# Kernel tuning notes

Measured on AMD Instinct MI355X. Metric: run time of the kernel, lower is better.

The kernel has to match this reference:

```python
import jax, jax.numpy as jnp
import numpy as np
from jax import lax

# 4D convolution (valid padding, stride 1) via XLA's rank-general conv.
# dimension_numbers: N=batch, C=channels, then 4 spatial axes H,W,D,T.
DN = ('NCHWDT', 'OIHWDT', 'NCHWDT')

def conv4d(x, w, b):
    y = lax.conv_general_dilated(x, w, window_strides=(1, 1, 1, 1),
                                 padding='VALID', dimension_numbers=DN)
    return y + b.reshape(1, -1, 1, 1, 1, 1)


def setup_inputs() -> dict:
    key = jax.random.key(0)
    ks = jax.random.split(key, 7)
    B = 128
    x = jax.random.normal(ks[0], (B, 1, 18, 18, 18, 18), dtype=jnp.float32)
    # conv4d(1, 5, 7): weight [out=5, in=1, 7,7,7,7]
    w1 = jax.random.normal(ks[1], (5, 1, 7, 7, 7, 7), dtype=jnp.float32) * 0.02
    b1 = jax.random.normal(ks[2], (5,), dtype=jnp.float32) * 0.02
    # conv4d(5, 10, 7): weight [10, 5, 7,7,7,7]
    w2 = jax.random.normal(ks[3], (10, 5, 7, 7, 7, 7), dtype=jnp.float32) * 0.02
    b2 = jax.random.normal(ks[4], (10,), dtype=jnp.float32) * 0.02
    # Linear(10 * 6**4, 1)
    feat = 10 * 6 ** 4  # 12960
    w_lin = jax.random.normal(ks[5], (1, feat), dtype=jnp.float32) * 0.02
    b_lin = jax.random.normal(ks[6], (1,), dtype=jnp.float32) * 0.02
    return {"x": x, "w1": w1, "b1": b1, "w2": w2, "b2": b2,
            "w_lin": w_lin, "b_lin": b_lin}


def reference(x, w1, b1, w2, b2, w_lin, b_lin):
    # head: conv4d -> ReLU -> conv4d -> ReLU
    h = jax.nn.relu(conv4d(x, w1, b1))          # [B, 5, 12,12,12,12]
    h = jax.nn.relu(conv4d(h, w2, b2))          # [B, 10, 6,6,6,6]
    # out: Flatten -> Dropout(eval: identity) -> Linear -> Sigmoid
    h = h.reshape(h.shape[0], -1)               # [B, 12960]
    logits = h @ w_lin.T + b_lin                 # [B, 1]
    return jax.nn.sigmoid(logits)
```

## Files before the change

### kernel.cpp

```cpp
#include <hip/hip_runtime.h>
#include <math.h>

typedef unsigned u32;
typedef _Float16 f16x8 __attribute__((ext_vector_type(8)));
typedef float    f32x16 __attribute__((ext_vector_type(16)));

static __device__ __forceinline__ u32 pack2(_Float16 a, _Float16 b) {
    union { _Float16 h[2]; u32 u; } v;
    v.h[0] = a; v.h[1] = b;
    return v.u;
}


__global__ __launch_bounds__(256) void pack_A1p(
    const float* __restrict__ w1, _Float16* __restrict__ A1)
{
    int i = blockIdx.x * 256 + threadIdx.x;
    if (i >= 9728) return;
    u32 outv = 0u;
    int kh = i / 1164, r = i % 1164;
    if (kh < 7 && r < 1148) {
        int kw = r / 164, r2 = r % 164;
        if (r2 < 140) {
            int kd = r2 / 20, r3 = r2 % 20;
            int oc = r3 / 4, j2 = r3 % 4;
            int j0 = 2 * j2, j1 = 2 * j2 + 1;
            const float* wb = w1 + oc * 2401 + kh * 343 + kw * 49 + kd * 7;
            _Float16 v0 = (j0 < 7) ? (_Float16)wb[j0] : (_Float16)0.f;
            _Float16 v1 = (j1 < 7) ? (_Float16)wb[j1] : (_Float16)0.f;
            outv = pack2(v0, v1);
        }
    }
    ((u32*)A1)[i] = outv;
}

__global__ __launch_bounds__(256) void pack_A2p(
    const float* __restrict__ w2, _Float16* __restrict__ A2)
{
    int i = blockIdx.x * 256 + threadIdx.x;
    if (i >= 79040) return;
    int ci = i / 15808, r = i % 15808;
    int kh = r / 1976, r2 = r % 1976;
    u32 outv = 0u;
    if (kh < 7 && r2 < 1960) {
        int kw = r2 / 280, r3 = r2 % 280;
        int kd = r3 / 40, r4 = r3 % 40;
        int oc = r4 / 4, j2 = r4 % 4;
        int j0 = 2 * j2, j1 = 2 * j2 + 1;
        const float* wb = w2 + oc * 12005 + ci * 2401 + kh * 343 + kw * 49 + kd * 7;
        _Float16 v0 = (j0 < 7) ? (_Float16)wb[j0] : (_Float16)0.f;
        _Float16 v1 = (j1 < 7) ? (_Float16)wb[j1] : (_Float16)0.f;
        outv = pack2(v0, v1);
    }
    ((u32*)A2)[i] = outv;
}

#define C1_SLAB 9360
#define C1_AOFF 9360
#define C1_LDS  (9360 + 9728)
__global__ __launch_bounds__(256, 2) void conv1_mfma(
    const float* __restrict__ x, const _Float16* __restrict__ A1,
    const float* __restrict__ b1, _Float16* __restrict__ h1)
{
    __shared__ u32 lds[C1_LDS];
    int tid = threadIdx.x;
    int lane = tid & 63;
    int wave = tid >> 6;
    int col = lane & 31;
    int g = lane >> 5;

    int bid = (int)blockIdx.x;
    int lbid = (bid & 7) * 192 + (bid >> 3);
    int OWp = lbid % 3;
    int OH = (lbid / 3) & 3;
    int b = lbid / 12;

    int qn[3], u_[3], od_[3], ot_[3];
    #pragma unroll
    for (int s = 0; s < 3; ++s) {
        int nt = wave + 4 * s;
        int n = (nt <= 8) ? nt * 32 + col : col;
        int u = n / 144, r2 = n % 144;
        int od = r2 / 12, ot = r2 % 12;
        u_[s] = u; od_[s] = od; ot_[s] = ot;
        qn[s] = (u * 36 + od) * 52 + ot * 4;
    }

    f32x16 acc0, acc1, acc2;
    #pragma unroll
    for (int q = 0; q < 16; ++q) { acc0[q] = 0.f; acc1[q] = 0.f; acc2[q] = 0.f; }

    const float* xbase = x + (size_t)b * 104976;
    int w10 = tid / 18, id18 = tid % 18;
    int iw = 4 * OWp + w10;
    bool stager = (tid < 180);

    int mc = (col < 30) ? col : 29;
    int am_dw = mc / 15, am_dh = (mc % 15) / 5, am_oc = mc % 5;
    int jadd = 4 * (col - mc);
    int vlane = 4 * am_oc - 164 * am_dw + jadd;
    int zbase = C1_AOFF + 8312 + vlane;
    bool eLo = (am_dw == 1);
    bool e3  = (am_dw == 1) && (g == 0);
    bool e24 = (am_dw == 0) && (g == 1);
    bool eHi = (am_dw == 0);

    float2 xr[9];
    {
        const uint4* asrc = (const uint4*)A1;
        uint4* adst = (uint4*)(lds + C1_AOFF);
        #pragma unroll
        for (int i = 0; i < 10; ++i) {
            int q = tid + 256 * i;
            if (q < 2432) adst[q] = asrc[q];
        }
        if (stager) {
            const float2* src = (const float2*)(xbase + (3 * OH) * 5832 + iw * 324 + id18 * 18);
            #pragma unroll
            for (int q = 0; q < 9; ++q) xr[q] = src[q];
        }
    }

    for (int se = 0; se < 9; ++se) {
        int kh = se - am_dh;
        int vbase = (kh >= 0 && kh < 7) ? (C1_AOFF + kh * 1164 + vlane) : zbase;

        __syncthreads();
        if (stager) {
            _Float16 h[19];
            #pragma unroll
            for (int q = 0; q < 9; ++q) { h[2*q] = (_Float16)xr[q].x; h[2*q+1] = (_Float16)xr[q].y; }
            h[18] = (_Float16)0.f;
            u32 e[9], o[9];
            #pragma unroll
            for (int q = 0; q < 9; ++q) e[q] = pack2(h[2*q], h[2*q+1]);
            #pragma unroll
            for (int q = 0; q < 9; ++q) o[q] = pack2(h[2*q+1], (q < 8) ? h[2*q+2] : h[18]);
            int base = tid * 52;
            #pragma unroll
            for (int ot = 0; ot < 12; ++ot) {
                uint4 w;
                if ((ot & 1) == 0) { const int q = ot >> 1;   w = (uint4){e[q], e[q+1], e[q+2], e[q+3]}; }
                else               { const int q = (ot-1)>>1; w = (uint4){o[q], o[q+1], o[q+2], o[q+3]}; }
                *(uint4*)(&lds[base + ot * 4]) = w;
            }
        }
        __syncthreads();

        if (se < 8 && stager) {
            const float2* src = (const float2*)(xbase + (3 * OH + se + 1) * 5832 + iw * 324 + id18 * 18);
            #pragma unroll
            for (int q = 0; q < 9; ++q) xr[q] = src[q];
        }

        #pragma unroll
        for (int k2 = 0; k2 < 28; ++k2) {
            const int t0 = 2 * k2, t1 = 2 * k2 + 1;
            const int c0 = ((t0 / 7) * 18 + (t0 % 7)) * 52;
            const int c1 = ((t1 / 7) * 18 + (t1 % 7)) * 52;
            const int ca0 = 164 * (t0 / 7) + 20 * (t0 % 7);
            const int ca1 = 164 * (t1 / 7) + 20 * (t1 % 7);
            int qoff = g ? c1 : c0;
            int ca   = g ? ca1 : ca0;
            int abase;
            if (k2 <= 2)       abase = eLo ? zbase : vbase;
            else if (k2 == 3)  abase = e3  ? zbase : vbase;
            else if (k2 == 24) abase = e24 ? zbase : vbase;
            else if (k2 >= 25) abase = eHi ? zbase : vbase;
            else               abase = vbase;
            f16x8 af = *(const f16x8*)(lds + abase + ca);
            f16x8 bf0 = *(const f16x8*)(lds + qn[0] + qoff);
            f16x8 bf1 = *(const f16x8*)(lds + qn[1] + qoff);
            acc0 = __builtin_amdgcn_mfma_f32_32x32x16_f16(af, bf0, acc0, 0, 0, 0);
            acc1 = __builtin_amdgcn_mfma_f32_32x32x16_f16(af, bf1, acc1, 0, 0, 0);
            if (wave == 0) {
                f16x8 bf2 = *(const f16x8*)(lds + qn[2] + qoff);
                acc2 = __builtin_amdgcn_mfma_f32_32x32x16_f16(af, bf2, acc2, 0, 0, 0);
            }
        }
    }

    #pragma unroll
    for (int s = 0; s < 3; ++s) {
        if (s == 2 && wave != 0) continue;
        f32x16 a = (s == 0) ? acc0 : ((s == 1) ? acc1 : acc2);
        int ow_b = 4 * OWp + 2 * u_[s];
        #pragma unroll
        for (int r = 0; r < 16; ++r) {
            const int m0 = (r & 3) + 8 * (r >> 2);
            const int m1 = m0 + 4;
            const int dw0 = m0 / 15, dh0 = (m0 % 15) / 5, oc0 = m0 % 5;
            const int dw1 = m1 / 15, dh1 = (m1 % 15) / 5, oc1 = m1 % 5;
            if (m1 >= 30 && g) continue;
            int dw = g ? dw1 : dw0;
            int dh = g ? dh1 : dh0;
            int oc = g ? oc1 : oc0;
            float bv = g ? b1[oc1] : b1[oc0];
            float v = fmaxf(a[r] + bv, 0.f);
            h1[(size_t)b * 103680 + oc * 20736 + (3 * OH + dh) * 1728
               + (ow_b + dw) * 144 + od_[s] * 12 + ot_[s]] = (_Float16)v;
        }
    }
}

#define C2_SLAB 4032
#define C2_AOFF 4032
#define C2_LDS  (4032 + 15808)
__global__ __launch_bounds__(256, 2) void conv2_mfma(
    const _Float16* __restrict__ h1, const _Float16* __restrict__ A2,
    _Float16* __restrict__ part)
{
    __shared__ u32 lds[C2_LDS];
    int tid = threadIdx.x;
    int lane = tid & 63;
    int wave = tid >> 6;
    int col = lane & 31;
    int g = lane >> 5;

    int bid = (int)blockIdx.x;
    int lbid = (bid & 7) * 160 + (bid >> 3);
    int ci = lbid % 5;
    int OH2 = (lbid / 5) & 1;
    int b = lbid / 10;

    int qn[2], n_[2];
    #pragma unroll
    for (int s = 0; s < 2; ++s) {
        int nt = wave + 4 * s;
        int n = nt * 32 + col;
        n_[s] = n;
        int nc = (n < 216) ? n : 215;
        int ow = nc / 36, rem = nc % 36;
        int od = rem / 6, ot = rem % 6;
        qn[s] = (ow * 12 + od) * 28 + ot * 4;
    }

    f32x16 acc0, acc1;
    #pragma unroll
    for (int q = 0; q < 16; ++q) { acc0[q] = 0.f; acc1[q] = 0.f; }

    const _Float16* hbase = h1 + (size_t)b * 103680 + ci * 20736;
    int iw = tid / 12, id12 = tid % 12;
    bool stager = (tid < 144);

    int mc = (col < 30) ? col : 29;
    int am_dh = mc / 10, am_oc = mc % 10;
    int jadd = 4 * (col - mc);
    int vlane = 4 * am_oc + jadd;
    int zb = C2_AOFF + 13832 + vlane;

    uint2 xr[3];
    {
        const uint4* asrc = (const uint4*)A2 + (size_t)ci * 3952;
        uint4* adst = (uint4*)(lds + C2_AOFF);
        #pragma unroll
        for (int i = 0; i < 16; ++i) {
            int q = tid + 256 * i;
            if (q < 3952) adst[q] = asrc[q];
        }
        if (stager) {
            const uint2* src = (const uint2*)(hbase + (3 * OH2) * 1728 + iw * 144 + id12 * 12);
            #pragma unroll
            for (int q = 0; q < 3; ++q) xr[q] = src[q];
        }
    }

    for (int she = 0; she < 9; ++she) {
        int kh = she - am_dh;
        int vb = (kh >= 0 && kh < 7) ? (C2_AOFF + kh * 1976 + vlane) : zb;

        __syncthreads();
        if (stager) {
            _Float16 h[14];
            *(uint2*)&h[0] = xr[0]; *(uint2*)&h[4] = xr[1]; *(uint2*)&h[8] = xr[2];
            h[12] = (_Float16)0.f;
            u32 e[6], o[6];
            #pragma unroll
            for (int q = 0; q < 6; ++q) e[q] = pack2(h[2*q], h[2*q+1]);
            #pragma unroll
            for (int q = 0; q < 6; ++q) o[q] = pack2(h[2*q+1], (q < 5) ? h[2*q+2] : h[12]);
            int base = tid * 28;
            #pragma unroll
            for (int ot = 0; ot < 6; ++ot) {
                uint4 w;
                if ((ot & 1) == 0) { const int q = ot >> 1;   w = (uint4){e[q], e[q+1], e[q+2], e[q+3]}; }
                else               { const int q = (ot-1)>>1; w = (uint4){o[q], o[q+1], o[q+2], o[q+3]}; }
                *(uint4*)(&lds[base + ot * 4]) = w;
            }
        }
        __syncthreads();

        if (she < 8 && stager) {
            const uint2* src = (const uint2*)(hbase + (3 * OH2 + she + 1) * 1728 + iw * 144 + id12 * 12);
            #pragma unroll
            for (int q = 0; q < 3; ++q) xr[q] = src[q];
        }

        #pragma unroll
        for (int k2 = 0; k2 < 25; ++k2) {
            const int t0 = 2 * k2, t1 = 2 * k2 + 1;
            const int c0 = ((t0 / 7) * 12 + (t0 % 7)) * 28;
            const int c1 = (t1 < 49) ? ((t1 / 7) * 12 + (t1 % 7)) * 28 : 0;
            const int a0 = 280 * (t0 / 7) + 40 * (t0 % 7);
            const int a1 = (t1 < 49) ? (280 * (t1 / 7) + 40 * (t1 % 7)) : 0;
            int qoff = g ? c1 : c0;
            int ca   = g ? a1 : a0;
            int ab = (k2 == 24 && g) ? zb : vb;
            f16x8 af = *(const f16x8*)(lds + ab + ca);
            f16x8 bf0 = *(const f16x8*)(lds + qn[0] + qoff);
            acc0 = __builtin_amdgcn_mfma_f32_32x32x16_f16(af, bf0, acc0, 0, 0, 0);
            if (wave < 3) {
                f16x8 bf1 = *(const f16x8*)(lds + qn[1] + qoff);
                acc1 = __builtin_amdgcn_mfma_f32_32x32x16_f16(af, bf1, acc1, 0, 0, 0);
            }
        }
    }

    #pragma unroll
    for (int s = 0; s < 2; ++s) {
        if (s == 1 && wave >= 3) continue;
        if (n_[s] >= 216) continue;
        f32x16 a = (s == 0) ? acc0 : acc1;
        #pragma unroll
        for (int r = 0; r < 16; ++r) {
            const int m0 = (r & 3) + 8 * (r >> 2);
            const int m1 = m0 + 4;
            const int dh0 = m0 / 10, oc0 = m0 % 10;
            const int dh1 = m1 / 10, oc1 = m1 % 10;
            if (m1 >= 30 && g) continue;
            int dh = g ? dh1 : dh0;
            int oc = g ? oc1 : oc0;
            int oh = 3 * OH2 + dh;
            part[((size_t)(ci * 768 + b * 6 + oh) * 10 + oc) * 216 + n_[s]] = (_Float16)a[r];
        }
    }
}

__global__ __launch_bounds__(256) void conv2_reduce(
    const _Float16* __restrict__ part, const float* __restrict__ b2,
    _Float16* __restrict__ h2)
{
    int flat = blockIdx.x * 256 + threadIdx.x;
    int n_loc = flat % 216;
    int t = flat / 216;
    int oc = t % 10;  t /= 10;
    int oh = t % 6;
    int b  = t / 6;
    float s = 0.f;
    #pragma unroll
    for (int ci = 0; ci < 5; ++ci)
        s += (float)part[((size_t)(ci * 768 + b * 6 + oh) * 10 + oc) * 216 + n_loc];
    s = fmaxf(s + b2[oc], 0.f);
    h2[(size_t)b * 12960 + oc * 1296 + oh * 216 + n_loc] = (_Float16)s;
}

__global__ __launch_bounds__(256) void linear_kernel(
    const _Float16* __restrict__ h2, const float* __restrict__ wl,
    const float* __restrict__ bl, float* __restrict__ out)
{
    int b = blockIdx.x;
    const _Float16* hb = h2 + (size_t)b * 12960;
    float s = 0.f;
    for (int i = threadIdx.x; i < 12960; i += 256)
        s += (float)hb[i] * wl[i];
    #pragma unroll
    for (int off = 32; off > 0; off >>= 1)
        s += __shfl_down(s, off, 64);
    __shared__ float wsum[4];
    int wave = threadIdx.x >> 6;
    if ((threadIdx.x & 63) == 0) wsum[wave] = s;
    __syncthreads();
    if (threadIdx.x == 0) {
        float tot = wsum[0] + wsum[1] + wsum[2] + wsum[3] + bl[0];
        out[b] = 1.f / (1.f + expf(-tot));
    }
}

extern "C" void kernel_launch(void* const* d_in, const int* in_sizes, int n_in,
                              void* d_out, int out_size, void* d_ws, size_t ws_size,
                              hipStream_t stream) {
    const float* x  = (const float*)d_in[0];
    const float* w1 = (const float*)d_in[1];
    const float* b1 = (const float*)d_in[2];
    const float* w2 = (const float*)d_in[3];
    const float* b2 = (const float*)d_in[4];
    const float* wl = (const float*)d_in[5];
    const float* bl = (const float*)d_in[6];
    float* out = (float*)d_out;

    _Float16* h1   = (_Float16*)d_ws;
    _Float16* A1   = h1 + 13271040;
    _Float16* A2   = A1 + 129024;
    _Float16* part = A2 + 576000;
    _Float16* h2   = part + 8294400;

    pack_A1p<<<38, 256, 0, stream>>>(w1, A1);
    pack_A2p<<<309, 256, 0, stream>>>(w2, A2);
    conv1_mfma<<<1536, 256, 0, stream>>>(x, A1, b1, h1);
    conv2_mfma<<<1280, 256, 0, stream>>>(h1, A2, part);
    conv2_reduce<<<6480, 256, 0, stream>>>(part, b2, h2);
    linear_kernel<<<128, 256, 0, stream>>>(h2, wl, bl, out);
}
```

Measured before the change: 237.4 us.

## Compute two output-H tiles per conv1 block to reuse staged input slabs

Each conv1 block now produces six output H rows instead of three. It keeps two accumulator sets (low and high), and each staged input H-slice feeds both tiles in the same k-loop. The B-fragment LDS reads are shared across the two MFMA chains, and the block count is halved. Input slice staging drops from 9 per 3 rows to 12 per 6 rows. The cost is double the accumulator registers, which puts pressure on occupancy under launch_bounds(256,2), and a grid of 768 blocks.

```diff
diff --git a/kernel.cpp b/kernel.cpp
--- a/kernel.cpp
+++ b/kernel.cpp
@@ -58,6 +58,45 @@
 #define C1_SLAB 9360
 #define C1_AOFF 9360
 #define C1_LDS  (9360 + 9728)
+
+#define C1_KLOOP(DOLO, DOHI)                                                          \
+    _Pragma("unroll")                                                                 \
+    for (int k2 = 0; k2 < 28; ++k2) {                                                 \
+        const int t0 = 2 * k2, t1 = 2 * k2 + 1;                                       \
+        const int c0 = ((t0 / 7) * 18 + (t0 % 7)) * 52;                               \
+        const int c1 = ((t1 / 7) * 18 + (t1 % 7)) * 52;                               \
+        const int ca0 = 164 * (t0 / 7) + 20 * (t0 % 7);                               \
+        const int ca1 = 164 * (t1 / 7) + 20 * (t1 % 7);                               \
+        int qoff = g ? c1 : c0;                                                       \
+        int ca   = g ? ca1 : ca0;                                                     \
+        bool z;                                                                       \
+        if (k2 <= 2)       z = eLo;                                                   \
+        else if (k2 == 3)  z = e3;                                                    \
+        else if (k2 == 24) z = e24;                                                   \
+        else if (k2 >= 25) z = eHi;                                                   \
+        else               z = false;                                                 \
+        f16x8 bf0 = *(const f16x8*)(lds + qn[0] + qoff);                              \
+        f16x8 bf1 = *(const f16x8*)(lds + qn[1] + qoff);                              \
+        f16x8 bf2;                                                                    \
+        if (wave == 0) bf2 = *(const f16x8*)(lds + qn[2] + qoff);                     \
+        if (DOLO) {                                                                   \
+            int ab = z ? zbase : vbL;                                                 \
+            f16x8 af = *(const f16x8*)(lds + ab + ca);                                \
+            accL[0] = __builtin_amdgcn_mfma_f32_32x32x16_f16(af, bf0, accL[0], 0,0,0);\
+            accL[1] = __builtin_amdgcn_mfma_f32_32x32x16_f16(af, bf1, accL[1], 0,0,0);\
+            if (wave == 0)                                                            \
+                accL[2] = __builtin_amdgcn_mfma_f32_32x32x16_f16(af, bf2, accL[2], 0,0,0);\
+        }                                                                             \
+        if (DOHI) {                                                                   \
+            int ab = z ? zbase : vbH;                                                 \
+            f16x8 af = *(const f16x8*)(lds + ab + ca);                                \
+            accH[0] = __builtin_amdgcn_mfma_f32_32x32x16_f16(af, bf0, accH[0], 0,0,0);\
+            accH[1] = __builtin_amdgcn_mfma_f32_32x32x16_f16(af, bf1, accH[1], 0,0,0);\
+            if (wave == 0)                                                            \
+                accH[2] = __builtin_amdgcn_mfma_f32_32x32x16_f16(af, bf2, accH[2], 0,0,0);\
+        }                                                                             \
+    }
+
 __global__ __launch_bounds__(256, 2) void conv1_mfma(
     const float* __restrict__ x, const _Float16* __restrict__ A1,
     const float* __restrict__ b1, _Float16* __restrict__ h1)
@@ -70,10 +109,10 @@
     int g = lane >> 5;
 
     int bid = (int)blockIdx.x;
-    int lbid = (bid & 7) * 192 + (bid >> 3);
+    int lbid = (bid & 7) * 96 + (bid >> 3);
     int OWp = lbid % 3;
-    int OH = (lbid / 3) & 3;
-    int b = lbid / 12;
+    int OH2 = (lbid / 3) & 1;
+    int b = lbid / 6;
 
     int qn[3], u_[3], od_[3], ot_[3];
     #pragma unroll
@@ -86,9 +125,11 @@
         qn[s] = (u * 36 + od) * 52 + ot * 4;
     }
 
-    f32x16 acc0, acc1, acc2;
-    #pragma unroll
-    for (int q = 0; q < 16; ++q) { acc0[q] = 0.f; acc1[q] = 0.f; acc2[q] = 0.f; }
+    f32x16 accL[3], accH[3];
+    #pragma unroll
+    for (int s = 0; s < 3; ++s)
+        #pragma unroll
+        for (int q = 0; q < 16; ++q) { accL[s][q] = 0.f; accH[s][q] = 0.f; }
 
     const float* xbase = x + (size_t)b * 104976;
     int w10 = tid / 18, id18 = tid % 18;
@@ -115,15 +156,17 @@
             if (q < 2432) adst[q] = asrc[q];
         }
         if (stager) {
-            const float2* src = (const float2*)(xbase + (3 * OH) * 5832 + iw * 324 + id18 * 18);
+            const float2* src = (const float2*)(xbase + (6 * OH2) * 5832 + iw * 324 + id18 * 18);
             #pragma unroll
             for (int q = 0; q < 9; ++q) xr[q] = src[q];
         }
     }
 
-    for (int se = 0; se < 9; ++se) {
-        int kh = se - am_dh;
-        int vbase = (kh >= 0 && kh < 7) ? (C1_AOFF + kh * 1164 + vlane) : zbase;
+    for (int p = 0; p < 12; ++p) {
+        int khL = p - am_dh;
+        int khH = khL - 3;
+        int vbL = (khL >= 0 && khL < 7) ? (C1_AOFF + khL * 1164 + vlane) : zbase;
+        int vbH = (khH >= 0 && khH < 7) ? (C1_AOFF + khH * 1164 + vlane) : zbase;
 
         __syncthreads();
         if (stager) {
@@ -147,58 +190,40 @@
         }
         __syncthreads();
 
-        if (se < 8 && stager) {
-            const float2* src = (const float2*)(xbase + (3 * OH + se + 1) * 5832 + iw * 324 + id18 * 18);
+        if (p < 11 && stager) {
+            const float2* src = (const float2*)(xbase + (6 * OH2 + p + 1) * 5832 + iw * 324 + id18 * 18);
             #pragma unroll
             for (int q = 0; q < 9; ++q) xr[q] = src[q];
         }
 
-        #pragma unroll
-        for (int k2 = 0; k2 < 28; ++k2) {
-            const int t0 = 2 * k2, t1 = 2 * k2 + 1;
-            const int c0 = ((t0 / 7) * 18 + (t0 % 7)) * 52;
-            const int c1 = ((t1 / 7) * 18 + (t1 % 7)) * 52;
-            const int ca0 = 164 * (t0 / 7) + 20 * (t0 % 7);
-            const int ca1 = 164 * (t1 / 7) + 20 * (t1 % 7);
-            int qoff = g ? c1 : c0;
-            int ca   = g ? ca1 : ca0;
-            int abase;
-            if (k2 <= 2)       abase = eLo ? zbase : vbase;
-            else if (k2 == 3)  abase = e3  ? zbase : vbase;
-            else if (k2 == 24) abase = e24 ? zbase : vbase;
-            else if (k2 >= 25) abase = eHi ? zbase : vbase;
-            else               abase = vbase;
-            f16x8 af = *(const f16x8*)(lds + abase + ca);
-            f16x8 bf0 = *(const f16x8*)(lds + qn[0] + qoff);
-            f16x8 bf1 = *(const f16x8*)(lds + qn[1] + qoff);
-            acc0 = __builtin_amdgcn_mfma_f32_32x32x16_f16(af, bf0, acc0, 0, 0, 0);
-            acc1 = __builtin_amdgcn_mfma_f32_32x32x16_f16(af, bf1, acc1, 0, 0, 0);
-            if (wave == 0) {
-                f16x8 bf2 = *(const f16x8*)(lds + qn[2] + qoff);
-                acc2 = __builtin_amdgcn_mfma_f32_32x32x16_f16(af, bf2, acc2, 0, 0, 0);
-            }
-        }
+        bool dolo = (p <= 8), dohi = (p >= 3);
+        if (dolo && dohi)      { C1_KLOOP(true,  true)  }
+        else if (dolo)         { C1_KLOOP(true,  false) }
+        else                   { C1_KLOOP(false, true)  }
     }
 
     #pragma unroll
     for (int s = 0; s < 3; ++s) {
         if (s == 2 && wave != 0) continue;
-        f32x16 a = (s == 0) ? acc0 : ((s == 1) ? acc1 : acc2);
         int ow_b = 4 * OWp + 2 * u_[s];
         #pragma unroll
-        for (int r = 0; r < 16; ++r) {
-            const int m0 = (r & 3) + 8 * (r >> 2);
-            const int m1 = m0 + 4;
-            const int dw0 = m0 / 15, dh0 = (m0 % 15) / 5, oc0 = m0 % 5;
-            const int dw1 = m1 / 15, dh1 = (m1 % 15) / 5, oc1 = m1 % 5;
-            if (m1 >= 30 && g) continue;
-            int dw = g ? dw1 : dw0;
-            int dh = g ? dh1 : dh0;
-            int oc = g ? oc1 : oc0;
-            float bv = g ? b1[oc1] : b1[oc0];
-            float v = fmaxf(a[r] + bv, 0.f);
-            h1[(size_t)b * 103680 + oc * 20736 + (3 * OH + dh) * 1728
-               + (ow_b + dw) * 144 + od_[s] * 12 + ot_[s]] = (_Float16)v;
+        for (int t = 0; t < 2; ++t) {
+            f32x16 a = (t == 0) ? accL[s] : accH[s];
+            #pragma unroll
+            for (int r = 0; r < 16; ++r) {
+                const int m0 = (r & 3) + 8 * (r >> 2);
+                const int m1 = m0 + 4;
+                const int dw0 = m0 / 15, dh0 = (m0 % 15) / 5, oc0 = m0 % 5;
+                const int dw1 = m1 / 15, dh1 = (m1 % 15) / 5, oc1 = m1 % 5;
+                if (m1 >= 30 && g) continue;
+                int dw = g ? dw1 : dw0;
+                int dh = (g ? dh1 : dh0) + 3 * t;
+                int oc = g ? oc1 : oc0;
+                float bv = g ? b1[oc1] : b1[oc0];
+                float v = fmaxf(a[r] + bv, 0.f);
+                h1[(size_t)b * 103680 + oc * 20736 + (6 * OH2 + dh) * 1728
+                   + (ow_b + dw) * 144 + od_[s] * 12 + ot_[s]] = (_Float16)v;
+            }
         }
     }
 }
@@ -396,7 +421,7 @@
 
     pack_A1p<<<38, 256, 0, stream>>>(w1, A1);
     pack_A2p<<<309, 256, 0, stream>>>(w2, A2);
-    conv1_mfma<<<1536, 256, 0, stream>>>(x, A1, b1, h1);
+    conv1_mfma<<<768, 256, 0, stream>>>(x, A1, b1, h1);
     conv2_mfma<<<1280, 256, 0, stream>>>(h1, A2, part);
     conv2_reduce<<<6480, 256, 0, stream>>>(part, b2, h2);
     linear_kernel<<<128, 256, 0, stream>>>(h2, wl, bl, out);
```

After: 282.9 us. +19.2%, slower.
